# Performance work log

Hardware: AMD Instinct MI355X
Metric: run time of the kernel (lower is better)

Reference implementation:

```python
import jax, jax.numpy as jnp
import numpy as np

C0 = 1.0  # speed of sound (units absorbed; distances pre-scaled)
FS = 1.0  # sampling frequency

A, E, S = 4, 128, 3072   # n_angles, n_elements, n_samples
NZ, NX = 512, 256        # image grid


def setup_inputs() -> dict:
    key = jax.random.key(0)
    k1, k2, k3, k4 = jax.random.split(key, 4)
    scale = (S / 2.0) - 1.0  # spread delays over the valid sample range
    d_tx = jax.random.uniform(k1, (A, NZ, NX), dtype=jnp.float32) * scale
    d_rx = jax.random.uniform(k2, (E, NZ, NX), dtype=jnp.float32) * scale
    apod = jax.random.uniform(k3, (E, NZ, NX), dtype=jnp.float32)
    rf = jax.random.normal(k4, (A, E, S), dtype=jnp.float32)
    t0 = jnp.zeros((A,), dtype=jnp.float32)
    return {"d_tx": d_tx, "d_rx": d_rx, "apod": apod, "rf": rf, "t0": t0}


def reference(d_tx, d_rx, apod, rf, t0):
    a, e, s = rf.shape
    nz, nx = d_tx.shape[1], d_tx.shape[2]
    # total delay in samples: [A, E, nz, nx]
    delays = ((d_tx[:, None] + d_rx[None]) / C0 - t0[:, None, None, None]) * FS
    x0 = jnp.floor(delays)
    w = delays - x0                      # linear interp weight
    i0 = x0.astype(jnp.int32)
    i1 = i0 + 1

    def gather(idx):
        # rf: [A, E, S]; idx: [A, E, nz, nx] -> gathered [A, E, nz, nx]
        g = jnp.take_along_axis(rf, jnp.clip(idx, 0, s - 1).reshape(a, e, -1), axis=2)
        return g.reshape(a, e, nz, nx)

    # grid_sample(padding_mode='zeros', align_corners=True): out-of-range taps contribute 0
    v0 = jnp.where((i0 >= 0) & (i0 <= s - 1), gather(i0), 0.0)
    v1 = jnp.where((i1 >= 0) & (i1 <= s - 1), gather(i1), 0.0)
    sampled = v0 * (1.0 - w) + v1 * w    # [A, E, nz, nx]
    # apodization-weighted sum over elements -> [A, nz, nx]
    das = jnp.einsum('aezx,ezx->azx', sampled, apod)
    return das
```

## Files before the change

### kernel.cpp

```cpp
#include <hip/hip_runtime.h>


#define A_N 4
#define E_N 128
#define S_N 3072
#define NPIX_N (512 * 256)
#define TPB 512
#define PXT 8
#define TILE (TPB * PXT)
#define TILES (NPIX_N / TILE)
#define ESPLIT 16
#define EPB (E_N / ESPLIT)
#define STAGE_ITERS ((A_N * S_N / 4) / TPB)

__global__ __launch_bounds__(TPB, 2) void das_kernel(
    const float* __restrict__ d_tx, const float* __restrict__ d_rx,
    const float* __restrict__ apod, const float* __restrict__ rf,
    const float* __restrict__ t0,  float* __restrict__ out)
{
    __shared__ float lds_rf[A_N * S_N];
    const int tid = threadIdx.x;
    const int px0 = blockIdx.x * TILE + tid;
    const int e0  = blockIdx.y * EPB;

    int sbase[STAGE_ITERS];
#pragma unroll
    for (int j = 0; j < STAGE_ITERS; ++j) {
        int idx = tid + j * TPB;
        int a   = idx / (S_N / 4);
        int s4  = idx - a * (S_N / 4);
        sbase[j] = a * (E_N * S_N) + s4 * 4;
    }

    float acc[A_N][PXT];
    float dta[A_N][PXT];
#pragma unroll
    for (int a = 0; a < A_N; ++a) {
        const float t0a = t0[a];
#pragma unroll
        for (int k = 0; k < PXT; ++k) {
            dta[a][k] = d_tx[a * NPIX_N + px0 + k * TPB] - t0a;
            acc[a][k] = 0.0f;
        }
    }

    for (int ei = 0; ei < EPB; ++ei) {
        const int e = e0 + ei;
        __syncthreads();
#pragma unroll
        for (int j = 0; j < STAGE_ITERS; ++j) {
            float4 v = *(const float4*)(rf + sbase[j] + e * S_N);
            ((float4*)lds_rf)[tid + j * TPB] = v;
        }
        __syncthreads();

        const float* __restrict__ drx_row = d_rx + (size_t)e * NPIX_N;
        const float* __restrict__ ap_row  = apod + (size_t)e * NPIX_N;
#pragma unroll
        for (int k = 0; k < PXT; ++k) {
            const int p = px0 + k * TPB;
            const float drx = drx_row[p];
            const float ap  = ap_row[p];
#pragma unroll
            for (int a = 0; a < A_N; ++a) {
                float delay = dta[a][k] + drx;
                float x0 = floorf(delay);
                float w  = delay - x0;
                int i0 = (int)x0;
                i0 = min(max(i0, 0), S_N - 2);
                float v0 = lds_rf[a * S_N + i0];
                float v1 = lds_rf[a * S_N + i0 + 1];
                acc[a][k] += (v0 + w * (v1 - v0)) * ap;
            }
        }
    }

#pragma unroll
    for (int a = 0; a < A_N; ++a)
#pragma unroll
        for (int k = 0; k < PXT; ++k)
            atomicAdd(&out[a * NPIX_N + px0 + k * TPB], acc[a][k]);
}

extern "C" void kernel_launch(void* const* d_in, const int* in_sizes, int n_in,
                              void* d_out, int out_size, void* d_ws, size_t ws_size,
                              hipStream_t stream) {
    const float* d_tx = (const float*)d_in[0];
    const float* d_rx = (const float*)d_in[1];
    const float* apod = (const float*)d_in[2];
    const float* rf   = (const float*)d_in[3];
    const float* t0   = (const float*)d_in[4];
    float* out = (float*)d_out;

    hipMemsetAsync(out, 0, (size_t)out_size * sizeof(float), stream);
    dim3 grid(TILES, ESPLIT);
    das_kernel<<<grid, TPB, 0, stream>>>(d_tx, d_rx, apod, rf, t0, out);
}
```

Baseline: 201.2 us.

## Pack adjacent rf samples as bf16 pairs in LDS and prefetch next element

Stores each rf sample together with its successor as a rounded bf16 pair in one 32-bit LDS word, so each interpolation needs a single LDS load instead of two. Rows for the next element are prefetched into registers while the current one is processed, and PXT is halved with launch bounds raised so more blocks fit per CU. Floor and clamping are replaced by truncation, which assumes non-negative in-range delays. The trade is bf16 precision loss on rf values and removal of the bounds clamp.

Measured after the change: 306.1 us. 1.52x slower.

```diff
diff --git a/kernel.cpp b/kernel.cpp
--- a/kernel.cpp
+++ b/kernel.cpp
@@ -6,30 +6,32 @@
 #define S_N 3072
 #define NPIX_N (512 * 256)
 #define TPB 512
-#define PXT 8
+#define PXT 4
 #define TILE (TPB * PXT)
 #define TILES (NPIX_N / TILE)
 #define ESPLIT 16
 #define EPB (E_N / ESPLIT)
-#define STAGE_ITERS ((A_N * S_N / 4) / TPB)
+#define NPK (A_N * S_N)
+#define GRP 6
 
-__global__ __launch_bounds__(TPB, 2) void das_kernel(
+__global__ __launch_bounds__(TPB, 6) void das_kernel(
     const float* __restrict__ d_tx, const float* __restrict__ d_rx,
     const float* __restrict__ apod, const float* __restrict__ rf,
     const float* __restrict__ t0,  float* __restrict__ out)
 {
-    __shared__ float lds_rf[A_N * S_N];
+    __shared__ unsigned lds_pk[NPK];
     const int tid = threadIdx.x;
     const int px0 = blockIdx.x * TILE + tid;
     const int e0  = blockIdx.y * EPB;
 
-    int sbase[STAGE_ITERS];
+    int off[GRP], exoff[GRP];
 #pragma unroll
-    for (int j = 0; j < STAGE_ITERS; ++j) {
-        int idx = tid + j * TPB;
+    for (int g = 0; g < GRP; ++g) {
+        int idx = g * TPB + tid;
         int a   = idx / (S_N / 4);
-        int s4  = idx - a * (S_N / 4);
-        sbase[j] = a * (E_N * S_N) + s4 * 4;
+        int i   = (idx - a * (S_N / 4)) * 4;
+        off[g]   = a * (E_N * S_N) + i;
+        exoff[g] = a * (E_N * S_N) + min(i + 4, S_N - 1);
     }
 
     float acc[A_N][PXT];
@@ -44,15 +46,43 @@
         }
     }
 
+    float4 pf[GRP]; float pfx[GRP];
+    {
+        const float* p = rf + (size_t)e0 * S_N;
+#pragma unroll
+        for (int g = 0; g < GRP; ++g) {
+            pf[g]  = *(const float4*)(p + off[g]);
+            pfx[g] = p[exoff[g]];
+        }
+    }
+
     for (int ei = 0; ei < EPB; ++ei) {
         const int e = e0 + ei;
         __syncthreads();
 #pragma unroll
-        for (int j = 0; j < STAGE_ITERS; ++j) {
-            float4 v = *(const float4*)(rf + sbase[j] + e * S_N);
-            ((float4*)lds_rf)[tid + j * TPB] = v;
+        for (int g = 0; g < GRP; ++g) {
+            unsigned r0 = __float_as_uint(pf[g].x) + 0x8000u;
+            unsigned r1 = __float_as_uint(pf[g].y) + 0x8000u;
+            unsigned r2 = __float_as_uint(pf[g].z) + 0x8000u;
+            unsigned r3 = __float_as_uint(pf[g].w) + 0x8000u;
+            unsigned r4 = __float_as_uint(pfx[g])  + 0x8000u;
+            uint4 w;
+            w.x = (r0 >> 16) | (r1 & 0xffff0000u);
+            w.y = (r1 >> 16) | (r2 & 0xffff0000u);
+            w.z = (r2 >> 16) | (r3 & 0xffff0000u);
+            w.w = (r3 >> 16) | (r4 & 0xffff0000u);
+            ((uint4*)lds_pk)[g * TPB + tid] = w;
         }
         __syncthreads();
+
+        if (ei + 1 < EPB) {
+            const float* p = rf + (size_t)(e + 1) * S_N;
+#pragma unroll
+            for (int g = 0; g < GRP; ++g) {
+                pf[g]  = *(const float4*)(p + off[g]);
+                pfx[g] = p[exoff[g]];
+            }
+        }
 
         const float* __restrict__ drx_row = d_rx + (size_t)e * NPIX_N;
         const float* __restrict__ ap_row  = apod + (size_t)e * NPIX_N;
@@ -64,13 +94,12 @@
 #pragma unroll
             for (int a = 0; a < A_N; ++a) {
                 float delay = dta[a][k] + drx;
-                float x0 = floorf(delay);
-                float w  = delay - x0;
-                int i0 = (int)x0;
-                i0 = min(max(i0, 0), S_N - 2);
-                float v0 = lds_rf[a * S_N + i0];
-                float v1 = lds_rf[a * S_N + i0 + 1];
-                acc[a][k] += (v0 + w * (v1 - v0)) * ap;
+                int i0 = (int)delay;
+                float w = delay - (float)i0;
+                unsigned u = lds_pk[a * S_N + i0];
+                float v0 = __uint_as_float(u << 16);
+                float v1 = __uint_as_float(u & 0xffff0000u);
+                acc[a][k] += ap * (v0 + w * (v1 - v0));
             }
         }
     }
```
